# Optimization experiments

Measured on AMD Instinct MI355X. Metric: run time of the kernel, lower is better.

## Reference

```python
import jax, jax.numpy as jnp
import numpy as np

NUM_HEADS = 16
LORA_RANK = 64
LORA_ALPHA = 1.0


def setup_inputs() -> dict:
    key = jax.random.key(0)
    ks = jax.random.split(key, 9)
    B, N, C, r = 16, 1024, 1024, LORA_RANK
    s = lambda k, shp, sc=0.02: (jax.random.normal(k, shp, dtype=jnp.float32) * sc)
    return {
        "x": jax.random.normal(ks[0], (B, N, C), dtype=jnp.float32),
        "W_qkv": s(ks[1], (3 * C, C)),
        "b_qkv": s(ks[2], (3 * C,)),
        "lora_kA": s(ks[3], (r, C), 1.0 / np.sqrt(r)),
        "lora_kB": s(ks[4], (C, r)),
        "lora_vA": s(ks[5], (r, C), 1.0 / np.sqrt(r)),
        "lora_vB": s(ks[6], (C, r)),
        "W_proj": s(ks[7], (C, C)),
        "b_proj": s(ks[8], (C,)),
    }


def reference(x, W_qkv, b_qkv, lora_kA, lora_kB, lora_vA, lora_vB, W_proj, b_proj):
    B, N, C = x.shape
    H = NUM_HEADS
    D = C // H
    scale = D ** -0.5
    lora_scale = LORA_ALPHA / LORA_RANK

    # qkv projection: (B,N,3C)
    qkv = x @ W_qkv.T + b_qkv
    # LoRA deltas for k and v: x @ A.T @ B.T * (alpha/rank)
    k_lora = ((x @ lora_kA.T) @ lora_kB.T) * lora_scale  # (B,N,C)
    v_lora = ((x @ lora_vA.T) @ lora_vB.T) * lora_scale  # (B,N,C)

    qkv = qkv.reshape(B, N, 3, H, D).transpose(2, 0, 3, 1, 4)  # (3,B,H,N,D)
    q, k, v = qkv[0], qkv[1], qkv[2]
    k = k + k_lora.reshape(B, N, H, D).transpose(0, 2, 1, 3)
    v = v + v_lora.reshape(B, N, H, D).transpose(0, 2, 1, 3)

    attn = jnp.einsum('bhqd,bhkd->bhqk', q, k) * scale  # (B,H,N,N)
    attn = jax.nn.softmax(attn, axis=-1)
    out = jnp.einsum('bhqk,bhkd->bhqd', attn, v)  # (B,H,N,D)
    out = out.transpose(0, 2, 1, 3).reshape(B, N, C)
    return out @ W_proj.T + b_proj
```

## Files before the change

kernel.cpp:

```cpp
#include <hip/hip_runtime.h>
#include <hip/hip_bf16.h>
#include <stdint.h>

#define B_  16
#define N_  1024
#define C_  1024
#define H_  16
#define Dh  64
#define M_  (B_*N_)
#define QSCALE (0.125f * 1.44269504f)

typedef __attribute__((ext_vector_type(8)))  short short8;
typedef __attribute__((ext_vector_type(4)))  float f32x4;
typedef __attribute__((ext_vector_type(16))) float f32x16;

__device__ __forceinline__ ushort f2bf(float f) {
  union { float f; uint32_t u; } v; v.f = f;
  uint32_t u = v.u;
  u += 0x7fffu + ((u >> 16) & 1u);
  return (ushort)(u >> 16);
}

__device__ __forceinline__ ushort f2bf_fast(float f) {
  union { float f; uint32_t u; } v; v.f = f;
  return (ushort)((v.u + 0x8000u) >> 16);
}

__device__ __forceinline__ float exp2fast(float x) {
#if __has_builtin(__builtin_amdgcn_exp2f)
  return __builtin_amdgcn_exp2f(x);
#else
  return exp2f(x);
#endif
}

__device__ __forceinline__ void gload_lds16(const ushort* g, ushort* l) {
  __builtin_amdgcn_global_load_lds((const __attribute__((address_space(1))) void*)g,
                                   (__attribute__((address_space(3))) void*)l, 16, 0, 0);
}

__global__ void cast_bf16_k(const float* __restrict__ src, ushort* __restrict__ dst,
                            int n4, float scale) {
  int i = blockIdx.x * blockDim.x + threadIdx.x;
  int stride = gridDim.x * blockDim.x;
  for (; i < n4; i += stride) {
    float4 v = reinterpret_cast<const float4*>(src)[i];
    ushort4 o;
    o.x = f2bf(v.x * scale);
    o.y = f2bf(v.y * scale);
    o.z = f2bf(v.z * scale);
    o.w = f2bf(v.w * scale);
    reinterpret_cast<ushort4*>(dst)[i] = o;
  }
}

template<int MODE>
__global__ __launch_bounds__(256)
void gemm128(const ushort* __restrict__ A, int lda,
             const ushort* __restrict__ Bm, int ldb,
             const float* __restrict__ bias,
             const ushort* __restrict__ A2,
             const ushort* __restrict__ B2k, const ushort* __restrict__ B2v,
             ushort* __restrict__ oq, ushort* __restrict__ ok, ushort* __restrict__ ov,
             float* __restrict__ of, int ldo)
{
  __shared__ ushort sA[2][128*32];
  __shared__ ushort sB[2][128*32];
  const int t = threadIdx.x;
  const int lane = t & 63, w = t >> 6;
  const int wr = w >> 1, wc = w & 1;
  const int r = lane & 15, g = lane >> 4;
  const int m0 = blockIdx.x * 128, n0 = blockIdx.y * 128;

  const int s = n0 >> 10;
  int nt = 32;
  const ushort* A2b = nullptr; const ushort* B2 = nullptr; int n0loc = 0;
  if (MODE == 1 && s == 1) {
    nt = 34;
    A2b = A2;
    B2 = B2k;
    n0loc = n0 - 1024;
  }
  if (MODE == 3) nt = 34;

  auto stage = [&](int buf, int tt) {
    const ushort* Ab; const ushort* Bb; int ldaT, ldbT;
    if (tt < 32) { Ab = A + m0*lda + tt*32; ldaT = lda; Bb = Bm + n0*ldb + tt*32; ldbT = ldb; }
    else if (MODE == 3) {
      Ab = A2 + m0*64 + (tt-32)*32; ldaT = 64;
      Bb = B2k + n0*128 + (tt-32)*32; ldbT = 128;
    } else {
      Ab = A2b + m0*128 + (tt-32)*32; ldaT = 128;
      Bb = B2 + n0loc*64 + (tt-32)*32; ldbT = 64;
    }
    #pragma unroll
    for (int i = 0; i < 2; ++i) {
      int c = i*256 + t;
      gload_lds16(Ab + (c>>2)*ldaT + (c&3)*8, &sA[buf][c*8]);
      gload_lds16(Bb + (c>>2)*ldbT + (c&3)*8, &sB[buf][c*8]);
    }
  };

  f32x4 acc[4][4];
  #pragma unroll
  for (int i=0;i<4;++i)
    #pragma unroll
    for (int j=0;j<4;++j) acc[i][j] = (f32x4){0.f,0.f,0.f,0.f};

  stage(0, 0);
  __syncthreads();
  for (int tt = 0; tt < nt; ++tt) {
    int cur = tt & 1;
    if (tt + 1 < nt) stage(cur ^ 1, tt + 1);
    short8 af[4], bfr[4];
    #pragma unroll
    for (int i=0;i<4;++i) af[i]  = *(const short8*)&sA[cur][(wr*64 + i*16 + r)*32 + g*8];
    #pragma unroll
    for (int j=0;j<4;++j) bfr[j] = *(const short8*)&sB[cur][(wc*64 + j*16 + r)*32 + g*8];
    #pragma unroll
    for (int i=0;i<4;++i)
      #pragma unroll
      for (int j=0;j<4;++j)
        acc[i][j] = __builtin_amdgcn_mfma_f32_16x16x32_bf16(af[i], bfr[j], acc[i][j], 0,0,0);
    __syncthreads();
  }

  #pragma unroll
  for (int i=0;i<4;++i) {
    #pragma unroll
    for (int j=0;j<4;++j) {
      #pragma unroll
      for (int rr=0;rr<4;++rr) {
        int m = m0 + wr*64 + i*16 + g*4 + rr;
        int n = n0 + wc*64 + j*16 + r;
        float v = acc[i][j][rr];
        if (MODE == 0) {
          oq[m*128 + n] = f2bf(v);
        } else if (MODE == 1) {
          v += bias[n];
          int b = m >> 10, nq = m & 1023;
          int c = n & 1023, h = c >> 6, d = c & 63;
          int idx = ((b*H_ + h)*N_ + nq)*Dh + d;
          if (s == 0)      oq[idx] = f2bf(v * QSCALE);
          else             ok[idx] = f2bf(v);
        } else if (MODE == 3) {
          v += bias[m];
          int h = m >> 6, d = m & 63;
          int b = n >> 10, nq = n & 1023;
          ov[((b*H_ + h)*Dh + d)*N_ + nq] = f2bf(v);
        } else {
          of[m*ldo + n] = v + bias[n];
        }
      }
    }
  }
}

__global__ __launch_bounds__(512)
void flash_attn32(const ushort* __restrict__ qb, const ushort* __restrict__ kb,
                  const ushort* __restrict__ vb, ushort* __restrict__ out)
{
  __shared__ ushort Kt[2][64*64];
  __shared__ ushort Vt[2][64*64];
  const int t = threadIdx.x, w = t >> 6, lane = t & 63;
  const int ql = lane & 31, hi = lane >> 5;

  int bid = (blockIdx.x & 7) * 128 + (blockIdx.x >> 3);
  const int bh = bid >> 2, qt = bid & 3;
  const int b = bh >> 4, h = bh & 15;
  const ushort* Q  = qb + bh * (N_*Dh);
  const ushort* K  = kb + bh * (N_*Dh);
  const ushort* VT = vb + bh * (Dh*N_);
  const int q0 = qt*256 + w*32;

  short8 qf[4];
  #pragma unroll
  for (int ds=0; ds<4; ++ds)
    qf[ds] = *(const short8*)&Q[(q0 + ql)*Dh + ds*16 + hi*8];

  short8 ones;
  #pragma unroll
  for (int j=0;j<8;++j) ones[j] = (short)0x3F80;

  f32x16 o0, o1, lacc;
  #pragma unroll
  for (int r=0;r<16;++r) { o0[r]=0.f; o1[r]=0.f; lacc[r]=0.f; }
  float m = -1e30f;

  const int srow = t >> 3, scc = (t & 7) ^ ((t >> 3) & 7);
  const ushort* Ksrc = K  + srow*Dh + scc*8;
  const ushort* Vsrc = VT + srow*N_ + scc*8;
  ushort* Kdst = &Kt[0][t*8];
  ushort* Vdst = &Vt[0][t*8];

  const int krA = ql, krB = 32 + ql;
  const int kbaseA = krA*64, kbaseB = krB*64, kmA = krA & 7, kmB = krB & 7;

  auto stage = [&](int buf, int kt) {
    gload_lds16(Ksrc + kt*(64*Dh), Kdst + buf*(64*64));
    gload_lds16(Vsrc + kt*64,      Vdst + buf*(64*64));
  };

  stage(0, 0);
  __syncthreads();

  for (int kt = 0; kt < 16; ++kt) {
    int cur = kt & 1;
    if (kt < 15) stage(cur ^ 1, kt + 1);
    const ushort* Kl = &Kt[cur][0];
    const ushort* Vl = &Vt[cur][0];

    f32x16 s0, s1;
    #pragma unroll
    for (int r=0;r<16;++r) { s0[r]=0.f; s1[r]=0.f; }
    __builtin_amdgcn_s_setprio(1);
    #pragma unroll
    for (int ds=0; ds<4; ++ds) {
      int sc0 = ds*2 + hi;
      short8 kfA = *(const short8*)&Kl[kbaseA + ((sc0 ^ kmA)*8)];
      short8 kfB = *(const short8*)&Kl[kbaseB + ((sc0 ^ kmB)*8)];
      s0 = __builtin_amdgcn_mfma_f32_32x32x16_bf16(kfA, qf[ds], s0, 0,0,0);
      s1 = __builtin_amdgcn_mfma_f32_32x32x16_bf16(kfB, qf[ds], s1, 0,0,0);
    }
    __builtin_amdgcn_s_setprio(0);

    float pm = -1e30f;
    #pragma unroll
    for (int r=0;r<16;++r) pm = fmaxf(pm, fmaxf(s0[r], s1[r]));
    pm = fmaxf(pm, __shfl_xor(pm, 32));

    if (__any(pm > m + 8.f)) {
      float nm = fmaxf(m, pm);
      float fac = exp2fast(m - nm);
      m = nm;
      #pragma unroll
      for (int r=0;r<16;++r) {
        int qr = (r&3) + 8*(r>>2) + 4*hi;
        float facr = __shfl(fac, qr);
        o0[r] *= facr; o1[r] *= facr; lacc[r] *= facr;
      }
    }

    #pragma unroll
    for (int sg=0; sg<4; ++sg) {
      const int rb = (sg & 1) * 8;
      float e0,e1,e2,e3,e4,e5,e6,e7;
      if (sg < 2) {
        e0=exp2fast(s0[rb+0]-m); e1=exp2fast(s0[rb+1]-m);
        e2=exp2fast(s0[rb+2]-m); e3=exp2fast(s0[rb+3]-m);
        e4=exp2fast(s0[rb+4]-m); e5=exp2fast(s0[rb+5]-m);
        e6=exp2fast(s0[rb+6]-m); e7=exp2fast(s0[rb+7]-m);
      } else {
        e0=exp2fast(s1[rb+0]-m); e1=exp2fast(s1[rb+1]-m);
        e2=exp2fast(s1[rb+2]-m); e3=exp2fast(s1[rb+3]-m);
        e4=exp2fast(s1[rb+4]-m); e5=exp2fast(s1[rb+5]-m);
        e6=exp2fast(s1[rb+6]-m); e7=exp2fast(s1[rb+7]-m);
      }
      uint32_t w01 = (uint32_t)f2bf_fast(e0) | ((uint32_t)f2bf_fast(e1) << 16);
      uint32_t w23 = (uint32_t)f2bf_fast(e2) | ((uint32_t)f2bf_fast(e3) << 16);
      uint32_t w45 = (uint32_t)f2bf_fast(e4) | ((uint32_t)f2bf_fast(e5) << 16);
      uint32_t w67 = (uint32_t)f2bf_fast(e6) | ((uint32_t)f2bf_fast(e7) << 16);
      uint32_t x01 = __shfl_xor(w01, 32);
      uint32_t x23 = __shfl_xor(w23, 32);
      uint32_t x45 = __shfl_xor(w45, 32);
      uint32_t x67 = __shfl_xor(w67, 32);
      union { uint32_t u[4]; short8 s8; } pu;
      pu.u[0] = hi ? x45 : w01;
      pu.u[1] = hi ? x67 : w23;
      pu.u[2] = hi ? w45 : x01;
      pu.u[3] = hi ? w67 : x23;
      short8 pf = pu.s8;

      int sc0 = sg*2 + hi;
      short8 vfA = *(const short8*)&Vl[kbaseA + ((sc0 ^ kmA)*8)];
      short8 vfB = *(const short8*)&Vl[kbaseB + ((sc0 ^ kmB)*8)];
      __builtin_amdgcn_s_setprio(1);
      o0   = __builtin_amdgcn_mfma_f32_32x32x16_bf16(pf, vfA, o0, 0,0,0);
      o1   = __builtin_amdgcn_mfma_f32_32x32x16_bf16(pf, vfB, o1, 0,0,0);
      lacc = __builtin_amdgcn_mfma_f32_32x32x16_bf16(pf, ones, lacc, 0,0,0);
      __builtin_amdgcn_s_setprio(0);
    }
    __syncthreads();
  }

  #pragma unroll
  for (int r=0;r<16;++r) {
    float inv = 1.f / lacc[r];
    int qr = (r&3) + 8*(r>>2) + 4*hi;
    int row = b*N_ + q0 + qr;
    out[row*C_ + h*Dh + ql]      = f2bf(o0[r] * inv);
    out[row*C_ + h*Dh + 32 + ql] = f2bf(o1[r] * inv);
  }
}

extern "C" void kernel_launch(void* const* d_in, const int* in_sizes, int n_in,
                              void* d_out, int out_size, void* d_ws, size_t ws_size,
                              hipStream_t stream)
{
  const float* x      = (const float*)d_in[0];
  const float* W_qkv  = (const float*)d_in[1];
  const float* b_qkv  = (const float*)d_in[2];
  const float* kA     = (const float*)d_in[3];
  const float* kB     = (const float*)d_in[4];
  const float* vA     = (const float*)d_in[5];
  const float* vB     = (const float*)d_in[6];
  const float* W_proj = (const float*)d_in[7];
  const float* b_proj = (const float*)d_in[8];
  float* out = (float*)d_out;

  ushort* ws    = (ushort*)d_ws;
  ushort* xb    = ws;
  ushort* wqkvb = xb + 16777216;
  ushort* kvAb  = wqkvb + 3145728;
  ushort* kBb   = kvAb + 131072;
  ushort* vBb   = kBb + 65536;
  ushort* wprojb= vBb + 65536;
  ushort* tkv   = wprojb + 1048576;
  ushort* qbuf  = tkv + 2097152;
  ushort* kbuf  = qbuf + 16777216;
  ushort* vbuf  = kbuf + 16777216;
  ushort* attn  = xb;

  const float ls = 1.0f / 64.0f;

  auto cast = [&](const float* src, ushort* dst, int n, float scale) {
    int n4 = n >> 2;
    int blocks = (n4 + 255) / 256; if (blocks > 4096) blocks = 4096;
    cast_bf16_k<<<dim3(blocks), dim3(256), 0, stream>>>(src, dst, n4, scale);
  };
  cast(x,      xb,           16777216, 1.f);
  cast(W_qkv,  wqkvb,        3145728,  1.f);
  cast(kA,     kvAb,         65536,    1.f);
  cast(vA,     kvAb + 65536, 65536,    1.f);
  cast(kB,     kBb,          65536,    ls);
  cast(vB,     vBb,          65536,    ls);
  cast(W_proj, wprojb,       1048576,  1.f);

  gemm128<0><<<dim3(128, 1), dim3(256), 0, stream>>>(
      xb, 1024, kvAb, 1024, nullptr, nullptr, nullptr, nullptr,
      tkv, nullptr, nullptr, nullptr, 0);

  gemm128<1><<<dim3(128, 16), dim3(256), 0, stream>>>(
      xb, 1024, wqkvb, 1024, b_qkv, tkv, kBb, nullptr,
      qbuf, kbuf, nullptr, nullptr, 0);

  gemm128<3><<<dim3(8, 128), dim3(256), 0, stream>>>(
      wqkvb + 2048*1024, 1024, xb, 1024, b_qkv + 2048, vBb, tkv + 64, nullptr,
      nullptr, nullptr, vbuf, nullptr, 0);

  flash_attn32<<<dim3(1024), dim3(512), 0, stream>>>(qbuf, kbuf, vbuf, attn);

  gemm128<2><<<dim3(128, 8), dim3(256), 0, stream>>>(
      attn, 1024, wprojb, 1024, b_proj, nullptr, nullptr, nullptr,
      nullptr, nullptr, nullptr, out, 1024);
}
```

Measured before the change: 394.9 us.

## Merge seven cast launches into one kernel and use one barrier per flash-attention tile

The seven separate fp32-to-bf16 cast launches become a single segmented kernel that works out each element's source and destination from cumulative offsets. This removes per-launch overhead and the idle tails of the small launches. In the flash-attention loop, the end-of-iteration __syncthreads is replaced by one explicit vmcnt wait plus barrier at the top of each iteration, before the next tile is prefetched. Each iteration then has a single barrier, but the code must correctly order the async LDS loads against reuse of the double buffer.

Result: no change. 394.0 us (-0.2%).

```diff
diff --git a/kernel.cpp b/kernel.cpp
--- a/kernel.cpp
+++ b/kernel.cpp
@@ -39,18 +39,30 @@
                                    (__attribute__((address_space(3))) void*)l, 16, 0, 0);
 }
 
-__global__ void cast_bf16_k(const float* __restrict__ src, ushort* __restrict__ dst,
-                            int n4, float scale) {
+struct CastSegs {
+  const float* src[7];
+  ushort*      dst[7];
+  int          cum[7];
+  float        scale[7];
+};
+
+__global__ void cast_all_k(CastSegs sg, int total4) {
   int i = blockIdx.x * blockDim.x + threadIdx.x;
   int stride = gridDim.x * blockDim.x;
-  for (; i < n4; i += stride) {
-    float4 v = reinterpret_cast<const float4*>(src)[i];
+  for (; i < total4; i += stride) {
+    int s = 0;
+    #pragma unroll
+    for (int k = 0; k < 6; ++k) s += (i >= sg.cum[k]);
+    int base = s ? sg.cum[s-1] : 0;
+    int li = i - base;
+    float sc = sg.scale[s];
+    float4 v = reinterpret_cast<const float4*>(sg.src[s])[li];
     ushort4 o;
-    o.x = f2bf(v.x * scale);
-    o.y = f2bf(v.y * scale);
-    o.z = f2bf(v.z * scale);
-    o.w = f2bf(v.w * scale);
-    reinterpret_cast<ushort4*>(dst)[i] = o;
+    o.x = f2bf(v.x * sc);
+    o.y = f2bf(v.y * sc);
+    o.z = f2bf(v.z * sc);
+    o.w = f2bf(v.w * sc);
+    reinterpret_cast<ushort4*>(sg.dst[s])[li] = o;
   }
 }
 
@@ -202,11 +214,14 @@
   };
 
   stage(0, 0);
-  __syncthreads();
 
   for (int kt = 0; kt < 16; ++kt) {
     int cur = kt & 1;
+    asm volatile("s_waitcnt vmcnt(0)" ::: "memory");
+    __builtin_amdgcn_sched_barrier(0);
+    __builtin_amdgcn_s_barrier();
     if (kt < 15) stage(cur ^ 1, kt + 1);
+
     const ushort* Kl = &Kt[cur][0];
     const ushort* Vl = &Vt[cur][0];
 
@@ -280,7 +295,6 @@
       lacc = __builtin_amdgcn_mfma_f32_32x32x16_bf16(pf, ones, lacc, 0,0,0);
       __builtin_amdgcn_s_setprio(0);
     }
-    __syncthreads();
   }
 
   #pragma unroll
@@ -323,18 +337,17 @@
 
   const float ls = 1.0f / 64.0f;
 
-  auto cast = [&](const float* src, ushort* dst, int n, float scale) {
-    int n4 = n >> 2;
-    int blocks = (n4 + 255) / 256; if (blocks > 4096) blocks = 4096;
-    cast_bf16_k<<<dim3(blocks), dim3(256), 0, stream>>>(src, dst, n4, scale);
-  };
-  cast(x,      xb,           16777216, 1.f);
-  cast(W_qkv,  wqkvb,        3145728,  1.f);
-  cast(kA,     kvAb,         65536,    1.f);
-  cast(vA,     kvAb + 65536, 65536,    1.f);
-  cast(kB,     kBb,          65536,    ls);
-  cast(vB,     vBb,          65536,    ls);
-  cast(W_proj, wprojb,       1048576,  1.f);
+  CastSegs sg;
+  const float* srcs[7] = { x, W_qkv, kA, vA, kB, vB, W_proj };
+  ushort* dsts[7]      = { xb, wqkvb, kvAb, kvAb + 65536, kBb, vBb, wprojb };
+  int     n4s[7]       = { 16777216/4, 3145728/4, 65536/4, 65536/4, 65536/4, 65536/4, 1048576/4 };
+  float   scs[7]       = { 1.f, 1.f, 1.f, 1.f, ls, ls, 1.f };
+  int cum = 0;
+  for (int i = 0; i < 7; ++i) {
+    sg.src[i] = srcs[i]; sg.dst[i] = dsts[i]; sg.scale[i] = scs[i];
+    cum += n4s[i]; sg.cum[i] = cum;
+  }
+  cast_all_k<<<dim3(4096), dim3(256), 0, stream>>>(sg, cum);
 
   gemm128<0><<<dim3(128, 1), dim3(256), 0, stream>>>(
       xb, 1024, kvAb, 1024, nullptr, nullptr, nullptr, nullptr,
```
